# Kernel optimization log

Measured on AMD Instinct MI355X. Metric: run time of the kernel, lower is better.

The kernel has to match this reference:

```python
import jax, jax.numpy as jnp
import numpy as np

N_EVENTS = 8388608
H_DIM, W_DIM = 480, 640
BIN_WIDTH = 0.01
A_INIT = 1e-4  # initial a_x = a_y


def setup_inputs() -> dict:
    key = jax.random.key(0)
    k1, k2, k3, k4 = jax.random.split(key, 4)
    x = jax.random.uniform(k1, (N_EVENTS,), dtype=jnp.float32) * W_DIM
    y = jax.random.uniform(k2, (N_EVENTS,), dtype=jnp.float32) * H_DIM
    ts = jax.random.uniform(k3, (N_EVENTS,), dtype=jnp.float32)  # seconds in [0,1)
    pol = jnp.where(jax.random.bernoulli(k4, 0.5, (N_EVENTS,)), 1.0, -1.0).astype(jnp.float32)
    params = jnp.array([A_INIT, A_INIT], dtype=jnp.float32)
    # num_bins is data-dependent in the torch source (Python int from tensor min/max);
    # compute it here on concrete data so the jitted reference uses a static shape.
    t_w = ts - params[0] * x - params[1] * y
    num_bins = int((float(t_w.max()) - float(t_w.min())) / BIN_WIDTH) + 1
    return {
        'params': params,
        'x_coords': x, 'y_coords': y, 'timestamps': ts, 'polarities': pol,
        'H': H_DIM, 'W': W_DIM, 'bin_width': BIN_WIDTH, 'num_bins': num_bins,
    }


def _forward(params, x_coords, y_coords, timestamps, polarities, H, W, bin_width, num_bins):
    # warp: shift timestamps by learned scan parameters
    t_warped = timestamps - params[0] * x_coords - params[1] * y_coords
    t_start = t_warped.min()
    t_norm = (t_warped - t_start) / jnp.float32(bin_width)
    t0 = jnp.floor(t_norm)
    wt = t_norm - t0  # bilinear-in-time weight
    t0c = jnp.clip(t0, 0, num_bins - 1).astype(jnp.int32)
    t1c = jnp.clip(t0 + 1.0, 0, num_bins - 1).astype(jnp.int32)
    xi = x_coords.astype(jnp.int32)
    yi = y_coords.astype(jnp.int32)
    valid = (xi >= 0) & (xi < W) & (yi >= 0) & (yi < H)
    # masked-weight scatter == torch's boolean filtering before scatter_add
    vmask = valid.astype(jnp.float32)
    spatial = jnp.where(valid, yi * W + xi, 0)
    fi0 = t0c * (H * W) + spatial
    fi1 = t1c * (H * W) + spatial
    w0 = (1.0 - wt) * polarities * vmask
    w1 = wt * polarities * vmask
    num_elements = num_bins * H * W
    flat = jnp.zeros((num_elements,), dtype=jnp.float32)
    flat = flat.at[fi0].add(w0).at[fi1].add(w1)
    event_tensor = flat.reshape(num_bins, H, W)
    # torch.var is unbiased (ddof=1)
    variances = jnp.var(event_tensor.reshape(num_bins, -1), axis=1, ddof=1)
    loss = jnp.mean(variances)
    return event_tensor, loss


def reference(params, x_coords, y_coords, timestamps, polarities, H, W, bin_width, num_bins):
    return _forward(params, x_coords, y_coords, timestamps, polarities, H, W, bin_width, num_bins)
```

## Files before the change

kernel.cpp:

```cpp
#include <hip/hip_runtime.h>

#define W_ 640
#define H_ 480
#define HW_ (W_ * H_)
#define VAR_SPLIT 8
#define MAXNB_T 124
#define NBAND 120
#define NTK 40
#define NT3 (NBAND * NTK)
#define FB 48
#define FT 32
#define FB2 128
#define FT2 64
#define PAD 16
#define OVF 131072
#define CPB 8


__device__ __forceinline__ unsigned fkey(float f) {
    unsigned u = __float_as_uint(f);
    return (u & 0x80000000u) ? ~u : (u | 0x80000000u);
}
__device__ __forceinline__ float finv(unsigned k) {
    unsigned u = (k & 0x80000000u) ? (k ^ 0x80000000u) : ~k;
    return __uint_as_float(u);
}
__device__ __forceinline__ float warp_t(float ts, float xf, float yf, float p0, float p1) {
    return __fsub_rn(__fsub_rn(ts, __fmul_rn(p0, xf)), __fmul_rn(p1, yf));
}

__device__ __forceinline__ void spill_rec(unsigned r, int band,
                                          int* ovfcur, uint2* ovfrecs) {
    int j = atomicAdd(ovfcur, 1);
    if (j < OVF) {
        int tk = min((int)((r >> 18) & 63u), NTK - 1);
        int pix = (int)((r >> 12) & 63u);
        int yi = band * 4 + tk / 10;
        int xi = (tk % 10) * 64 + pix;
        int b = (int)((r >> 24) & 127u);
        float wt = __fmul_rn((float)(r & 4095u), 2.44140625e-4f);
        unsigned px = ((unsigned)b << 20) | (unsigned)(yi * W_ + xi) | (r & 0x80000000u);
        ovfrecs[j] = make_uint2(px, __float_as_uint(wt));
    }
}

__global__ void k_init(float* __restrict__ out, int n4, unsigned* __restrict__ minbits,
                       int* __restrict__ ovfcur, double* __restrict__ sums, int nsums,
                       int* __restrict__ curs, int ncur) {
    int tid = blockIdx.x * blockDim.x + threadIdx.x;
    int stride = gridDim.x * blockDim.x;
    float4* o4 = (float4*)out;
    float4 z = make_float4(0.f, 0.f, 0.f, 0.f);
    for (int i = tid; i < n4; i += stride) o4[i] = z;
    for (int i = tid; i < ncur; i += stride) curs[i] = 0;
    if (tid == 0) { *minbits = 0xFFFFFFFFu; *ovfcur = 0; }
    if (tid < nsums) sums[tid] = 0.0;
}

__global__ void k_min(const float* __restrict__ x, const float* __restrict__ y,
                      const float* __restrict__ ts, const float* __restrict__ params,
                      int n, unsigned* __restrict__ minbits) {
    float p0 = params[0], p1 = params[1];
    int tid = blockIdx.x * blockDim.x + threadIdx.x;
    int stride = gridDim.x * blockDim.x;
    int n4 = n >> 2;
    const float4* x4 = (const float4*)x;
    const float4* y4 = (const float4*)y;
    const float4* t4 = (const float4*)ts;
    unsigned k = 0xFFFFFFFFu;
    for (int i = tid; i < n4; i += stride) {
        float4 xv = x4[i], yv = y4[i], tv = t4[i];
        unsigned k0 = fkey(warp_t(tv.x, xv.x, yv.x, p0, p1));
        unsigned k1 = fkey(warp_t(tv.y, xv.y, yv.y, p0, p1));
        unsigned k2 = fkey(warp_t(tv.z, xv.z, yv.z, p0, p1));
        unsigned k3 = fkey(warp_t(tv.w, xv.w, yv.w, p0, p1));
        unsigned ka = min(k0, k1), kb = min(k2, k3);
        k = min(k, min(ka, kb));
    }
    for (int i = (n4 << 2) + tid; i < n; i += stride)
        k = min(k, fkey(warp_t(ts[i], x[i], y[i], p0, p1)));
    #pragma unroll
    for (int off = 32; off > 0; off >>= 1) {
        unsigned o = __shfl_down(k, off, 64);
        k = (o < k) ? o : k;
    }
    if ((threadIdx.x & 63) == 0) atomicMin(minbits, k);
}

__global__ void __launch_bounds__(256) k_pass1(
        const float* __restrict__ x, const float* __restrict__ y,
        const float* __restrict__ ts, const float* __restrict__ pol,
        const float* __restrict__ params, const float* __restrict__ bwp,
        int n, int nb, int cap1, int per, const unsigned* __restrict__ minbits,
        int* __restrict__ gcur, unsigned* __restrict__ recs1,
        int* __restrict__ ovfcur, uint2* __restrict__ ovfrecs) {
    __shared__ unsigned buf[NBAND][FB];
    __shared__ int cnt[NBAND];
    float p0 = params[0], p1 = params[1], bw = bwp[0];
    float tstart = finv(*minbits);
    float nbm1 = (float)(nb - 1);
    for (int t = threadIdx.x; t < NBAND; t += 256) cnt[t] = 0;
    __syncthreads();
    int lo = blockIdx.x * per;
    int hi = min(n, lo + per);
    int total = (hi > lo) ? (hi - lo) : 0;
    int nf4 = total >> 2;
    const float4* x4 = (const float4*)(x + lo);
    const float4* y4 = (const float4*)(y + lo);
    const float4* t4 = (const float4*)(ts + lo);
    const float4* p4 = (const float4*)(pol + lo);
    int wave = threadIdx.x >> 6, lane = threadIdx.x & 63;

    auto proc = [&](float xf, float yf, float tf, float pf) {
        int xi = (int)xf, yi = (int)yf;
        if (xi >= 0 && xi < W_ && yi >= 0 && yi < H_) {
            float tn = __fdiv_rn(__fsub_rn(warp_t(tf, xf, yf, p0, p1), tstart), bw);
            float t0f = floorf(tn);
            float wt = __fsub_rn(tn, t0f);
            int b = (int)fminf(fmaxf(t0f, 0.0f), nbm1);
            unsigned sgn = __float_as_uint(pf) & 0x80000000u;
            int band = yi >> 2;
            unsigned tk = (unsigned)((yi & 3) * 10 + (xi >> 6));
            unsigned pix = (unsigned)(xi & 63);
            unsigned wq = (unsigned)__fmul_rn(wt, 4096.0f);
            unsigned rec = sgn | ((unsigned)b << 24) | (tk << 18) | (pix << 12) | wq;
            int pos = atomicAdd(&cnt[band], 1);
            if (pos < FB) buf[band][pos] = rec;
            else {
                int j = atomicAdd(ovfcur, 1);
                if (j < OVF) {
                    unsigned px = ((unsigned)b << 20) | (unsigned)(yi * W_ + xi) | sgn;
                    ovfrecs[j] = make_uint2(px, __float_as_uint(wt));
                }
            }
        }
    };
    auto flush = [&](int thresh) {
        for (int bb = wave; bb < NBAND; bb += 4) {
            int c = min(cnt[bb], FB);
            if (c >= thresh) {
                int base = 0;
                if (lane == 0) base = atomicAdd(&gcur[bb * PAD], c);
                base = __shfl(base, 0, 64);
                for (int j = lane; j < c; j += 64) {
                    unsigned r = buf[bb][j];
                    int idx = base + j;
                    if (idx < cap1) recs1[(size_t)bb * cap1 + idx] = r;
                    else spill_rec(r, bb, ovfcur, ovfrecs);
                }
                if (lane == 0) cnt[bb] = 0;
            }
        }
    };

    int iters = (nf4 + 255) >> 8;
    for (int it = 0; it < iters; it++) {
        int i4 = (it << 8) + (int)threadIdx.x;
        bool valid = (i4 < nf4);
        float4 xv, yv, tv, pv;
        if (valid) { xv = x4[i4]; yv = y4[i4]; tv = t4[i4]; pv = p4[i4]; }
        if (valid) {
            proc(xv.x, yv.x, tv.x, pv.x);
            proc(xv.y, yv.y, tv.y, pv.y);
            proc(xv.z, yv.z, tv.z, pv.z);
            proc(xv.w, yv.w, tv.w, pv.w);
        }
        __syncthreads();
        flush(FT);
        __syncthreads();
    }
    int tbase = lo + (nf4 << 2);
    int trem = hi - tbase;
    if ((int)threadIdx.x < trem) {
        int i = tbase + (int)threadIdx.x;
        proc(x[i], y[i], ts[i], pol[i]);
    }
    __syncthreads();
    flush(1);
}

__global__ void __launch_bounds__(256) k_pass2(
        const unsigned* __restrict__ recs1, const int* __restrict__ gcur,
        int cap1, int cap2, int* __restrict__ tcur, unsigned* __restrict__ recs2,
        int* __restrict__ ovfcur, uint2* __restrict__ ovfrecs) {
    __shared__ unsigned buf[NTK][FB2];
    __shared__ int cnt[NTK];
    int band = blockIdx.x / CPB;
    int chunk = blockIdx.x % CPB;
    int c1 = min(gcur[band * PAD], cap1);
    int chunklen = (((c1 + CPB - 1) / CPB) + 3) & ~3;
    int start = chunk * chunklen;
    int end = min(start + chunklen, c1);
    const unsigned* seg = recs1 + (size_t)band * cap1;
    for (int t = threadIdx.x; t < NTK; t += 256) cnt[t] = 0;
    __syncthreads();
    int iters = (end > start) ? ((end - start + 1023) >> 10) : 0;
    int wave = threadIdx.x >> 6, lane = threadIdx.x & 63;
    for (int it = 0; it < iters; it++) {
        int idx = start + (it << 10) + (int)threadIdx.x * 4;
        unsigned r4[4];
        int m = 0;
        if (idx + 4 <= end) {
            uint4 q = *(const uint4*)&seg[idx];
            r4[0] = q.x; r4[1] = q.y; r4[2] = q.z; r4[3] = q.w; m = 4;
        } else {
            for (; idx + m < end && m < 4; m++) r4[m] = seg[idx + m];
        }
        #pragma unroll
        for (int k = 0; k < 4; k++) {
            if (k < m) {
                unsigned r = r4[k];
                int tx = min((int)((r >> 18) & 63u), NTK - 1);
                int pos = atomicAdd(&cnt[tx], 1);
                if (pos < FB2) buf[tx][pos] = r;
                else spill_rec(r, band, ovfcur, ovfrecs);
            }
        }
        __syncthreads();
        bool last = (it == iters - 1);
        for (int bb = wave; bb < NTK; bb += 4) {
            int c = min(cnt[bb], FB2);
            if (c >= (last ? 1 : FT2)) {
                int base = 0;
                if (lane == 0) base = atomicAdd(&tcur[(band * NTK + bb) * PAD], c);
                base = __shfl(base, 0, 64);
                for (int j = lane; j < c; j += 64) {
                    unsigned r = buf[bb][j];
                    int o = base + j;
                    if (o < cap2) recs2[(size_t)(band * NTK + bb) * cap2 + o] = r;
                    else spill_rec(r, band, ovfcur, ovfrecs);
                }
                if (lane == 0) cnt[bb] = 0;
            }
        }
        __syncthreads();
    }
}

__global__ void __launch_bounds__(256) k_accum6(
        const unsigned* __restrict__ recs2, const int* __restrict__ tcur,
        int nb, int cap2, float* __restrict__ out, double2* __restrict__ part2) {
    extern __shared__ float acc[];
    int T = blockIdx.x;
    int band = T / NTK, tk = T % NTK;
    int yy = band * 4 + tk / 10;
    int x0 = (tk % 10) * 64;
    int nacc4 = nb << 4;
    float4* acc4 = (float4*)acc;
    float4 z4 = make_float4(0.f, 0.f, 0.f, 0.f);
    for (int i = threadIdx.x; i < nacc4; i += 256) acc4[i] = z4;
    __syncthreads();
    int c2 = min(tcur[T * PAD], cap2);
    const unsigned* seg = recs2 + (size_t)T * cap2;
    int iters = (c2 + 1023) >> 10;
    for (int it = 0; it < iters; it++) {
        int idx = (it << 10) + (int)threadIdx.x * 4;
        unsigned r4[4];
        int m = 0;
        if (idx + 4 <= c2) {
            uint4 q = *(const uint4*)&seg[idx];
            r4[0] = q.x; r4[1] = q.y; r4[2] = q.z; r4[3] = q.w; m = 4;
        } else {
            for (; idx + m < c2 && m < 4; m++) r4[m] = seg[idx + m];
        }
        #pragma unroll
        for (int k = 0; k < 4; k++) {
            if (k < m) {
                unsigned r = r4[k];
                int b = min((int)((r >> 24) & 127u), nb - 1);
                int b1 = min(b + 1, nb - 1);
                int pix = (int)((r >> 12) & 63u);
                unsigned sgn = r & 0x80000000u;
                float wt = __fmul_rn((float)(r & 4095u), 2.44140625e-4f);
                float w0 = __uint_as_float(__float_as_uint(__fsub_rn(1.0f, wt)) ^ sgn);
                float w1 = __uint_as_float(__float_as_uint(wt) ^ sgn);
                atomicAdd(&acc[(b << 6) + pix], w0);
                atomicAdd(&acc[(b1 << 6) + pix], w1);
            }
        }
    }
    __syncthreads();
    size_t rowbase = (size_t)yy * W_ + x0;
    for (int i = threadIdx.x; i < nacc4; i += 256) {
        int b = i >> 4;
        int q = i & 15;
        *(float4*)&out[(size_t)b * HW_ + rowbase + (q << 2)] = acc4[i];
    }
    int t = threadIdx.x;
    if (t < 2 * nb) {
        int b = t >> 1, half = t & 1;
        double s = 0.0, ss = 0.0;
        int basei = (b << 6) + (half << 5);
        for (int jj = 0; jj < 32; jj++) {
            float v = acc[basei + ((jj + b) & 31)];
            double dv = (double)v;
            s += dv; ss += dv * dv;
        }
        part2[(size_t)T * (2 * nb) + t] = make_double2(s, ss);
    }
}

__global__ void __launch_bounds__(256) k_redsum(
        const double2* __restrict__ part2, int nb,
        double* __restrict__ sumv, double* __restrict__ sumsq) {
    int b = blockIdx.x;
    double s = 0.0, ss = 0.0;
    for (int i = threadIdx.x; i < NT3; i += 256) {
        double2 a = part2[(size_t)i * (2 * nb) + 2 * b];
        double2 c = part2[(size_t)i * (2 * nb) + 2 * b + 1];
        s += a.x + c.x; ss += a.y + c.y;
    }
    #pragma unroll
    for (int off = 32; off > 0; off >>= 1) {
        s += __shfl_down(s, off, 64);
        ss += __shfl_down(ss, off, 64);
    }
    __shared__ double sb[4], sb2[4];
    int wave = threadIdx.x >> 6, lane = threadIdx.x & 63;
    if (lane == 0) { sb[wave] = s; sb2[wave] = ss; }
    __syncthreads();
    if (threadIdx.x == 0) {
        for (int i = 1; i < 4; i++) { s += sb[i]; ss += sb2[i]; }
        sumv[b] = s; sumsq[b] = ss;
    }
}

__global__ void __launch_bounds__(256) k_accum2(
        const unsigned* __restrict__ recs1, const int* __restrict__ gcur,
        int nb, int cap1, float* __restrict__ out,
        double* __restrict__ sumv, double* __restrict__ sumsq) {
    extern __shared__ float acc[];
    int h = blockIdx.x;
    int xcd = h & 7;
    int j = h >> 3;
    int kk2 = j / NTK;
    int tk = j % NTK;
    int ry = xcd + 8 * kk2;
    int nacc = nb << 6;
    for (int i = threadIdx.x; i < nacc; i += 256) acc[i] = 0.f;
    __syncthreads();
    int c1 = min(gcur[ry * PAD], cap1);
    const unsigned* seg = recs1 + (size_t)ry * cap1;
    unsigned tku = (unsigned)tk;
    int iters = (c1 + 1023) >> 10;
    for (int it = 0; it < iters; it++) {
        int idx = (it << 10) + (int)threadIdx.x * 4;
        unsigned r4[4];
        int m = 0;
        if (idx + 4 <= c1) {
            uint4 q = *(const uint4*)&seg[idx];
            r4[0] = q.x; r4[1] = q.y; r4[2] = q.z; r4[3] = q.w; m = 4;
        } else {
            for (; idx + m < c1 && m < 4; m++) r4[m] = seg[idx + m];
        }
        #pragma unroll
        for (int k = 0; k < 4; k++) {
            if (k < m) {
                unsigned r = r4[k];
                if (((r >> 18) & 63u) == tku) {
                    int b = min((int)((r >> 24) & 127u), nb - 1);
                    int b1 = min(b + 1, nb - 1);
                    int pix = (int)((r >> 12) & 63u);
                    unsigned sgn = r & 0x80000000u;
                    float wt = __fmul_rn((float)(r & 4095u), 2.44140625e-4f);
                    float w0 = __uint_as_float(__float_as_uint(__fsub_rn(1.0f, wt)) ^ sgn);
                    float w1 = __uint_as_float(__float_as_uint(wt) ^ sgn);
                    atomicAdd(&acc[(b << 6) + pix], w0);
                    atomicAdd(&acc[(b1 << 6) + pix], w1);
                }
            }
        }
    }
    __syncthreads();
    int yy = ry * 4 + tk / 10;
    int x0 = (tk % 10) * 64;
    for (int i = threadIdx.x; i < nacc; i += 256) {
        int b = i >> 6, p = i & 63;
        out[(size_t)b * HW_ + (size_t)yy * W_ + x0 + p] = acc[i];
    }
    if ((int)threadIdx.x < nb) {
        int b = threadIdx.x;
        double s = 0.0, ss = 0.0;
        for (int j2 = 0; j2 < 64; j2++) {
            float v = acc[(b << 6) + ((j2 + b) & 63)];
            double dv = (double)v;
            s += dv; ss += dv * dv;
        }
        atomicAdd(&sumv[b], s);
        atomicAdd(&sumsq[b], ss);
    }
}

__global__ void k_ovf(const uint2* __restrict__ ovfrecs, const int* __restrict__ ovfcur,
                      int nb, float* __restrict__ out,
                      double* __restrict__ sumv, double* __restrict__ sumsq) {
    int m = min(*ovfcur, OVF);
    int tid = blockIdx.x * blockDim.x + threadIdx.x;
    int stride = gridDim.x * blockDim.x;
    for (int i = tid; i < m; i += stride) {
        uint2 r = ovfrecs[i];
        unsigned sgn = r.x & 0x80000000u;
        int b = (int)((r.x >> 20) & 511u);
        int sp = (int)(r.x & 0x7FFFFu);
        b = min(b, nb - 1); sp = min(sp, HW_ - 1);
        int b1 = min(b + 1, nb - 1);
        float wt = __uint_as_float(r.y);
        float w0 = __uint_as_float(__float_as_uint(__fsub_rn(1.0f, wt)) ^ sgn);
        float w1 = __uint_as_float(r.y ^ sgn);
        float o0 = unsafeAtomicAdd(out + (size_t)b * HW_ + sp, w0);
        atomicAdd(&sumv[b], (double)w0);
        atomicAdd(&sumsq[b], (double)w0 * ((double)w0 + 2.0 * (double)o0));
        float o1 = unsafeAtomicAdd(out + (size_t)b1 * HW_ + sp, w1);
        atomicAdd(&sumv[b1], (double)w1);
        atomicAdd(&sumsq[b1], (double)w1 * ((double)w1 + 2.0 * (double)o1));
    }
}

__global__ void k_scatter(const float* __restrict__ x, const float* __restrict__ y,
                          const float* __restrict__ ts, const float* __restrict__ pol,
                          const float* __restrict__ params, const float* __restrict__ bwp,
                          int n, int nb, const unsigned* __restrict__ minbits,
                          float* __restrict__ out) {
    float p0 = params[0], p1 = params[1];
    float bw = bwp[0];
    float tstart = finv(*minbits);
    float nbm1 = (float)(nb - 1);
    int tid = blockIdx.x * blockDim.x + threadIdx.x;
    int stride = gridDim.x * blockDim.x;
    for (int i = tid; i < n; i += stride) {
        float xf = x[i], yf = y[i];
        float tn = __fdiv_rn(__fsub_rn(warp_t(ts[i], xf, yf, p0, p1), tstart), bw);
        float t0f = floorf(tn);
        float wt = __fsub_rn(tn, t0f);
        int t0c = (int)fminf(fmaxf(t0f, 0.0f), nbm1);
        int t1c = (int)fminf(fmaxf(__fadd_rn(t0f, 1.0f), 0.0f), nbm1);
        int xi = (int)xf, yi = (int)yf;
        if (xi >= 0 && xi < W_ && yi >= 0 && yi < H_) {
            int sp = yi * W_ + xi;
            float p = pol[i];
            float w0 = __fmul_rn(__fsub_rn(1.0f, wt), p);
            float w1 = __fmul_rn(wt, p);
            unsafeAtomicAdd(&out[(size_t)t0c * HW_ + sp], w0);
            unsafeAtomicAdd(&out[(size_t)t1c * HW_ + sp], w1);
        }
    }
}

__global__ void k_sums(const float* __restrict__ out, double* __restrict__ sumv,
                       double* __restrict__ sumsq) {
    int b = blockIdx.x / VAR_SPLIT;
    int part = blockIdx.x % VAR_SPLIT;
    const int chunk = HW_ / VAR_SPLIT;
    const float* p = out + (size_t)b * HW_ + (size_t)part * chunk;
    double s = 0.0, ss = 0.0;
    for (int i = threadIdx.x; i < chunk; i += blockDim.x) {
        double v = (double)p[i];
        s += v; ss += v * v;
    }
    #pragma unroll
    for (int off = 32; off > 0; off >>= 1) {
        s += __shfl_down(s, off, 64);
        ss += __shfl_down(ss, off, 64);
    }
    __shared__ double sb[8], sb2[8];
    int wave = threadIdx.x >> 6, lane = threadIdx.x & 63;
    if (lane == 0) { sb[wave] = s; sb2[wave] = ss; }
    __syncthreads();
    if (threadIdx.x == 0) {
        int nw = blockDim.x >> 6;
        for (int i = 1; i < nw; i++) { s += sb[i]; ss += sb2[i]; }
        atomicAdd(&sumv[b], s);
        atomicAdd(&sumsq[b], ss);
    }
}

__global__ void k_final(const double* __restrict__ sumv, const double* __restrict__ sumsq,
                        int nb, float* __restrict__ loss) {
    double acc = 0.0;
    const double n = (double)HW_;
    for (int b = threadIdx.x; b < nb; b += blockDim.x) {
        double s = sumv[b], ss = sumsq[b];
        acc += (ss - s * s / n) / (n - 1.0);
    }
    #pragma unroll
    for (int off = 32; off > 0; off >>= 1) acc += __shfl_down(acc, off, 64);
    __shared__ double sb[8];
    int wave = threadIdx.x >> 6, lane = threadIdx.x & 63;
    if (lane == 0) sb[wave] = acc;
    __syncthreads();
    if (threadIdx.x == 0) {
        int nw = blockDim.x >> 6;
        for (int i = 1; i < nw; i++) acc += sb[i];
        *loss = (float)(acc / (double)nb);
    }
}

extern "C" void kernel_launch(void* const* d_in, const int* in_sizes, int n_in,
                              void* d_out, int out_size, void* d_ws, size_t ws_size,
                              hipStream_t stream) {
    const float* params = (const float*)d_in[0];
    const float* x      = (const float*)d_in[1];
    const float* y      = (const float*)d_in[2];
    const float* ts     = (const float*)d_in[3];
    const float* pol    = (const float*)d_in[4];
    const float* bwp    = (const float*)d_in[7];

    int n  = in_sizes[1];
    int nb = (out_size - 1) / HW_;
    float* out = (float*)d_out;

    size_t off_sums  = 128;
    size_t off_gcur  = (off_sums + 16ULL * nb + 63) & ~(size_t)63;
    size_t off_tcur  = off_gcur + 4ULL * NBAND * PAD;
    size_t off_part  = (off_tcur + 4ULL * NT3 * PAD + 63) & ~(size_t)63;
    size_t off_ovfr  = (off_part + 16ULL * 2 * nb * NT3 + 63) & ~(size_t)63;
    size_t off_recs1 = (off_ovfr + 8ULL * OVF + 63) & ~(size_t)63;

    unsigned* minbits = (unsigned*)d_ws;
    int*      ovfcur  = (int*)((char*)d_ws + 64);
    double*   sumv    = (double*)((char*)d_ws + off_sums);
    double*   sumsq   = sumv + nb;
    int*      gcur    = (int*)((char*)d_ws + off_gcur);
    int*      tcur    = (int*)((char*)d_ws + off_tcur);
    double2*  part2   = (double2*)((char*)d_ws + off_part);
    uint2*    ovfrecs = (uint2*)((char*)d_ws + off_ovfr);
    unsigned* recs1   = (unsigned*)((char*)d_ws + off_recs1);

    long long mean1 = (long long)n / NBAND;
    long long mean2 = (long long)n / NT3;

    long long cap1e = (mean1 + mean1 / 8 + 2048) & ~3LL;
    size_t off_recs2 = (off_recs1 + 4ULL * NBAND * cap1e + 63) & ~(size_t)63;
    unsigned* recs2 = (unsigned*)((char*)d_ws + off_recs2);
    long long avail2 = (ws_size > off_recs2)
                       ? (long long)((ws_size - off_recs2) / (4ULL * NT3)) : 0;
    long long cap2min = mean2 + mean2 / 8 + 128;
    long long cap2max = 2 * mean2 + 512;
    long long cap2ll = ((avail2 < cap2max) ? avail2 : cap2max) & ~3LL;
    bool exact = (n > 0) && (nb >= 1) && (nb <= MAXNB_T) && (cap2ll >= cap2min);

    long long avail1 = (ws_size > off_recs1)
                       ? (long long)((ws_size - off_recs1) / (4ULL * NBAND)) : 0;
    long long cap1f_max = 2 * mean1 + 4096;
    long long cap1fll = ((avail1 < cap1f_max) ? avail1 : cap1f_max) & ~3LL;
    bool filter = !exact && (n > 0) && (nb >= 1) && (nb <= MAXNB_T) &&
                  (cap1fll >= mean1 + mean1 / 12 + 2048);

    int cap1 = (int)(exact ? cap1e : cap1fll);
    int cap2 = (int)cap2ll;

    int n_tensor = nb * HW_;
    int n4 = (exact || filter) ? 0 : (n_tensor >> 2);

    const int BLK = 256;
    const int G1 = 1280;
    const int ITBLK = 1024;
    int per = (((n + G1 - 1) / G1) + ITBLK - 1) / ITBLK * ITBLK;
    int g1used = (n + per - 1) / per;

    hipLaunchKernelGGL(k_init, dim3(512), dim3(BLK), 0, stream,
                       out, n4, minbits, ovfcur, sumv, 2 * nb,
                       gcur, NBAND * PAD + NT3 * PAD);
    hipLaunchKernelGGL(k_min, dim3(2048), dim3(BLK), 0, stream,
                       x, y, ts, params, n, minbits);

    if (exact) {
        hipLaunchKernelGGL(k_pass1, dim3(g1used), dim3(BLK), 0, stream,
                           x, y, ts, pol, params, bwp, n, nb, cap1, per, minbits,
                           gcur, recs1, ovfcur, ovfrecs);
        hipLaunchKernelGGL(k_pass2, dim3(NBAND * CPB), dim3(BLK), 0, stream,
                           recs1, gcur, cap1, cap2, tcur, recs2, ovfcur, ovfrecs);
        hipLaunchKernelGGL(k_accum6, dim3(NT3), dim3(BLK), (size_t)nb * 64 * 4, stream,
                           recs2, tcur, nb, cap2, out, part2);
        hipLaunchKernelGGL(k_redsum, dim3(nb), dim3(BLK), 0, stream,
                           part2, nb, sumv, sumsq);
        hipLaunchKernelGGL(k_ovf, dim3(64), dim3(BLK), 0, stream,
                           ovfrecs, ovfcur, nb, out, sumv, sumsq);
    } else if (filter) {
        hipLaunchKernelGGL(k_pass1, dim3(g1used), dim3(BLK), 0, stream,
                           x, y, ts, pol, params, bwp, n, nb, cap1, per, minbits,
                           gcur, recs1, ovfcur, ovfrecs);
        hipLaunchKernelGGL(k_accum2, dim3(NT3), dim3(BLK), (size_t)nb * 64 * 4, stream,
                           recs1, gcur, nb, cap1, out, sumv, sumsq);
        hipLaunchKernelGGL(k_ovf, dim3(64), dim3(BLK), 0, stream,
                           ovfrecs, ovfcur, nb, out, sumv, sumsq);
    } else {
        hipLaunchKernelGGL(k_scatter, dim3(2048), dim3(BLK), 0, stream,
                           x, y, ts, pol, params, bwp, n, nb, minbits, out);
        hipLaunchKernelGGL(k_sums, dim3(nb * VAR_SPLIT), dim3(BLK), 0, stream,
                           out, sumv, sumsq);
    }

    hipLaunchKernelGGL(k_final, dim3(1), dim3(BLK), 0, stream,
                       sumv, sumsq, nb, out + n_tensor);
}
```

Before: 372.4 us.

## Bucket by time bin in pass2 and accumulate full 4-row bands per bin

Pass2 now splits each 4-row band's records by time bin rather than by 64-pixel tile. The accumulate kernel runs one block per (bin, band) with a 4x640 shared accumulator and pulls records from the current bin and the previous bin to add the w1 weights. The aim is a smaller shared footprint for better occupancy and fully contiguous output writes. The global atomicMin for the warped-time minimum becomes a two-stage block reduction, and the filter fallback path is removed. Each record is now read twice, and the smaller per-bin buffers may spill more records to the overflow path.

```diff
diff --git a/kernel.cpp b/kernel.cpp
--- a/kernel.cpp
+++ b/kernel.cpp
@@ -6,15 +6,14 @@
 #define VAR_SPLIT 8
 #define MAXNB_T 124
 #define NBAND 120
-#define NTK 40
-#define NT3 (NBAND * NTK)
 #define FB 48
 #define FT 32
-#define FB2 128
-#define FT2 64
+#define FB2 64
+#define FT2 32
 #define PAD 16
 #define OVF 131072
 #define CPB 8
+#define G0MIN 1280
 
 
 __device__ __forceinline__ unsigned fkey(float f) {
@@ -33,10 +32,9 @@
                                           int* ovfcur, uint2* ovfrecs) {
     int j = atomicAdd(ovfcur, 1);
     if (j < OVF) {
-        int tk = min((int)((r >> 18) & 63u), NTK - 1);
-        int pix = (int)((r >> 12) & 63u);
-        int yi = band * 4 + tk / 10;
-        int xi = (tk % 10) * 64 + pix;
+        int pix12 = (int)((r >> 12) & 4095u);
+        int yi = band * 4 + pix12 / W_;
+        int xi = pix12 % W_;
         int b = (int)((r >> 24) & 127u);
         float wt = __fmul_rn((float)(r & 4095u), 2.44140625e-4f);
         unsigned px = ((unsigned)b << 20) | (unsigned)(yi * W_ + xi) | (r & 0x80000000u);
@@ -57,9 +55,10 @@
     if (tid < nsums) sums[tid] = 0.0;
 }
 
-__global__ void k_min(const float* __restrict__ x, const float* __restrict__ y,
-                      const float* __restrict__ ts, const float* __restrict__ params,
-                      int n, unsigned* __restrict__ minbits) {
+__global__ void __launch_bounds__(256) k_min(
+        const float* __restrict__ x, const float* __restrict__ y,
+        const float* __restrict__ ts, const float* __restrict__ params,
+        int n, unsigned* __restrict__ minarr) {
     float p0 = params[0], p1 = params[1];
     int tid = blockIdx.x * blockDim.x + threadIdx.x;
     int stride = gridDim.x * blockDim.x;
@@ -74,17 +73,46 @@
         unsigned k1 = fkey(warp_t(tv.y, xv.y, yv.y, p0, p1));
         unsigned k2 = fkey(warp_t(tv.z, xv.z, yv.z, p0, p1));
         unsigned k3 = fkey(warp_t(tv.w, xv.w, yv.w, p0, p1));
-        unsigned ka = min(k0, k1), kb = min(k2, k3);
-        k = min(k, min(ka, kb));
+        k = min(k, min(min(k0, k1), min(k2, k3)));
     }
     for (int i = (n4 << 2) + tid; i < n; i += stride)
         k = min(k, fkey(warp_t(ts[i], x[i], y[i], p0, p1)));
     #pragma unroll
     for (int off = 32; off > 0; off >>= 1) {
         unsigned o = __shfl_down(k, off, 64);
-        k = (o < k) ? o : k;
-    }
-    if ((threadIdx.x & 63) == 0) atomicMin(minbits, k);
+        k = min(k, o);
+    }
+    __shared__ unsigned sb[4];
+    int wave = threadIdx.x >> 6, lane = threadIdx.x & 63;
+    if (lane == 0) sb[wave] = k;
+    __syncthreads();
+    if (threadIdx.x == 0) {
+        unsigned m = sb[0];
+        #pragma unroll
+        for (int i = 1; i < 4; i++) m = min(m, sb[i]);
+        minarr[blockIdx.x] = m;
+    }
+}
+
+__global__ void k_minred(const unsigned* __restrict__ minarr, int g,
+                         unsigned* __restrict__ minbits) {
+    unsigned k = 0xFFFFFFFFu;
+    for (int i = threadIdx.x; i < g; i += 256) k = min(k, minarr[i]);
+    #pragma unroll
+    for (int off = 32; off > 0; off >>= 1) {
+        unsigned o = __shfl_down(k, off, 64);
+        k = min(k, o);
+    }
+    __shared__ unsigned sb[4];
+    int wave = threadIdx.x >> 6, lane = threadIdx.x & 63;
+    if (lane == 0) sb[wave] = k;
+    __syncthreads();
+    if (threadIdx.x == 0) {
+        unsigned m = sb[0];
+        #pragma unroll
+        for (int i = 1; i < 4; i++) m = min(m, sb[i]);
+        *minbits = m;
+    }
 }
 
 __global__ void __launch_bounds__(256) k_pass1(
@@ -120,10 +148,9 @@
             int b = (int)fminf(fmaxf(t0f, 0.0f), nbm1);
             unsigned sgn = __float_as_uint(pf) & 0x80000000u;
             int band = yi >> 2;
-            unsigned tk = (unsigned)((yi & 3) * 10 + (xi >> 6));
-            unsigned pix = (unsigned)(xi & 63);
+            unsigned pix12 = (unsigned)((yi & 3) * W_ + xi);
             unsigned wq = (unsigned)__fmul_rn(wt, 4096.0f);
-            unsigned rec = sgn | ((unsigned)b << 24) | (tk << 18) | (pix << 12) | wq;
+            unsigned rec = sgn | ((unsigned)b << 24) | (pix12 << 12) | wq;
             int pos = atomicAdd(&cnt[band], 1);
             if (pos < FB) buf[band][pos] = rec;
             else {
@@ -181,10 +208,11 @@
 
 __global__ void __launch_bounds__(256) k_pass2(
         const unsigned* __restrict__ recs1, const int* __restrict__ gcur,
-        int cap1, int cap2, int* __restrict__ tcur, unsigned* __restrict__ recs2,
+        int nb, int cap1, int cap2, int* __restrict__ tcur,
+        unsigned* __restrict__ recs2,
         int* __restrict__ ovfcur, uint2* __restrict__ ovfrecs) {
-    __shared__ unsigned buf[NTK][FB2];
-    __shared__ int cnt[NTK];
+    __shared__ unsigned buf[MAXNB_T][FB2];
+    __shared__ int cnt[MAXNB_T];
     int band = blockIdx.x / CPB;
     int chunk = blockIdx.x % CPB;
     int c1 = min(gcur[band * PAD], cap1);
@@ -192,7 +220,7 @@
     int start = chunk * chunklen;
     int end = min(start + chunklen, c1);
     const unsigned* seg = recs1 + (size_t)band * cap1;
-    for (int t = threadIdx.x; t < NTK; t += 256) cnt[t] = 0;
+    for (int t = threadIdx.x; t < nb; t += 256) cnt[t] = 0;
     __syncthreads();
     int iters = (end > start) ? ((end - start + 1023) >> 10) : 0;
     int wave = threadIdx.x >> 6, lane = threadIdx.x & 63;
@@ -210,24 +238,24 @@
         for (int k = 0; k < 4; k++) {
             if (k < m) {
                 unsigned r = r4[k];
-                int tx = min((int)((r >> 18) & 63u), NTK - 1);
-                int pos = atomicAdd(&cnt[tx], 1);
-                if (pos < FB2) buf[tx][pos] = r;
+                int bi = min((int)((r >> 24) & 127u), nb - 1);
+                int pos = atomicAdd(&cnt[bi], 1);
+                if (pos < FB2) buf[bi][pos] = r;
                 else spill_rec(r, band, ovfcur, ovfrecs);
             }
         }
         __syncthreads();
         bool last = (it == iters - 1);
-        for (int bb = wave; bb < NTK; bb += 4) {
+        for (int bb = wave; bb < nb; bb += 4) {
             int c = min(cnt[bb], FB2);
             if (c >= (last ? 1 : FT2)) {
                 int base = 0;
-                if (lane == 0) base = atomicAdd(&tcur[(band * NTK + bb) * PAD], c);
+                if (lane == 0) base = atomicAdd(&tcur[(band * nb + bb) * PAD], c);
                 base = __shfl(base, 0, 64);
                 for (int j = lane; j < c; j += 64) {
                     unsigned r = buf[bb][j];
                     int o = base + j;
-                    if (o < cap2) recs2[(size_t)(band * NTK + bb) * cap2 + o] = r;
+                    if (o < cap2) recs2[(size_t)(band * nb + bb) * cap2 + o] = r;
                     else spill_rec(r, band, ovfcur, ovfrecs);
                 }
                 if (lane == 0) cnt[bb] = 0;
@@ -237,157 +265,102 @@
     }
 }
 
-__global__ void __launch_bounds__(256) k_accum6(
+__global__ void __launch_bounds__(256) k_accum8(
         const unsigned* __restrict__ recs2, const int* __restrict__ tcur,
-        int nb, int cap2, float* __restrict__ out, double2* __restrict__ part2) {
-    extern __shared__ float acc[];
-    int T = blockIdx.x;
-    int band = T / NTK, tk = T % NTK;
-    int yy = band * 4 + tk / 10;
-    int x0 = (tk % 10) * 64;
-    int nacc4 = nb << 4;
+        int nb, int cap2, float* __restrict__ out, double2* __restrict__ part) {
+    __shared__ float acc[4 * W_];
+    __shared__ double sb[4], sb2[4];
+    int blk = blockIdx.x;
+    int band = blk % NBAND;
+    int b = blk / NBAND;
     float4* acc4 = (float4*)acc;
     float4 z4 = make_float4(0.f, 0.f, 0.f, 0.f);
-    for (int i = threadIdx.x; i < nacc4; i += 256) acc4[i] = z4;
-    __syncthreads();
-    int c2 = min(tcur[T * PAD], cap2);
-    const unsigned* seg = recs2 + (size_t)T * cap2;
-    int iters = (c2 + 1023) >> 10;
-    for (int it = 0; it < iters; it++) {
-        int idx = (it << 10) + (int)threadIdx.x * 4;
-        unsigned r4[4];
-        int m = 0;
-        if (idx + 4 <= c2) {
-            uint4 q = *(const uint4*)&seg[idx];
-            r4[0] = q.x; r4[1] = q.y; r4[2] = q.z; r4[3] = q.w; m = 4;
-        } else {
-            for (; idx + m < c2 && m < 4; m++) r4[m] = seg[idx + m];
-        }
-        #pragma unroll
-        for (int k = 0; k < 4; k++) {
-            if (k < m) {
-                unsigned r = r4[k];
-                int b = min((int)((r >> 24) & 127u), nb - 1);
-                int b1 = min(b + 1, nb - 1);
-                int pix = (int)((r >> 12) & 63u);
-                unsigned sgn = r & 0x80000000u;
-                float wt = __fmul_rn((float)(r & 4095u), 2.44140625e-4f);
-                float w0 = __uint_as_float(__float_as_uint(__fsub_rn(1.0f, wt)) ^ sgn);
-                float w1 = __uint_as_float(__float_as_uint(wt) ^ sgn);
-                atomicAdd(&acc[(b << 6) + pix], w0);
-                atomicAdd(&acc[(b1 << 6) + pix], w1);
+    for (int i = threadIdx.x; i < 640; i += 256) acc4[i] = z4;
+    __syncthreads();
+
+    auto apply = [&](const unsigned* seg, int c, bool addw0, bool addw1) {
+        int iters = (c + 1023) >> 10;
+        for (int it = 0; it < iters; it++) {
+            int idx = (it << 10) + (int)threadIdx.x * 4;
+            unsigned r4[4];
+            int m = 0;
+            if (idx + 4 <= c) {
+                uint4 q = *(const uint4*)&seg[idx];
+                r4[0] = q.x; r4[1] = q.y; r4[2] = q.z; r4[3] = q.w; m = 4;
+            } else {
+                for (; idx + m < c && m < 4; m++) r4[m] = seg[idx + m];
             }
-        }
-    }
-    __syncthreads();
-    size_t rowbase = (size_t)yy * W_ + x0;
-    for (int i = threadIdx.x; i < nacc4; i += 256) {
-        int b = i >> 4;
-        int q = i & 15;
-        *(float4*)&out[(size_t)b * HW_ + rowbase + (q << 2)] = acc4[i];
-    }
-    int t = threadIdx.x;
-    if (t < 2 * nb) {
-        int b = t >> 1, half = t & 1;
-        double s = 0.0, ss = 0.0;
-        int basei = (b << 6) + (half << 5);
-        for (int jj = 0; jj < 32; jj++) {
-            float v = acc[basei + ((jj + b) & 31)];
-            double dv = (double)v;
-            s += dv; ss += dv * dv;
-        }
-        part2[(size_t)T * (2 * nb) + t] = make_double2(s, ss);
-    }
-}
-
-__global__ void __launch_bounds__(256) k_redsum(
-        const double2* __restrict__ part2, int nb,
-        double* __restrict__ sumv, double* __restrict__ sumsq) {
-    int b = blockIdx.x;
+            #pragma unroll
+            for (int k = 0; k < 4; k++) {
+                if (k < m) {
+                    unsigned r = r4[k];
+                    int pix = min((int)((r >> 12) & 4095u), 4 * W_ - 1);
+                    unsigned sgn = r & 0x80000000u;
+                    float wt = __fmul_rn((float)(r & 4095u), 2.44140625e-4f);
+                    if (addw0) {
+                        float w0 = __uint_as_float(__float_as_uint(__fsub_rn(1.0f, wt)) ^ sgn);
+                        atomicAdd(&acc[pix], w0);
+                    }
+                    if (addw1) {
+                        float w1 = __uint_as_float(__float_as_uint(wt) ^ sgn);
+                        atomicAdd(&acc[pix], w1);
+                    }
+                }
+            }
+        }
+    };
+
+    int base = band * nb;
+    int cb = min(tcur[(base + b) * PAD], cap2);
+    apply(recs2 + (size_t)(base + b) * cap2, cb, true, b == nb - 1);
+    if (b > 0) {
+        int cm = min(tcur[(base + b - 1) * PAD], cap2);
+        apply(recs2 + (size_t)(base + b - 1) * cap2, cm, false, true);
+    }
+    __syncthreads();
+    float4* dst4 = (float4*)(out + (size_t)b * HW_ + (size_t)band * 4 * W_);
+    for (int i = threadIdx.x; i < 640; i += 256) dst4[i] = acc4[i];
     double s = 0.0, ss = 0.0;
-    for (int i = threadIdx.x; i < NT3; i += 256) {
-        double2 a = part2[(size_t)i * (2 * nb) + 2 * b];
-        double2 c = part2[(size_t)i * (2 * nb) + 2 * b + 1];
-        s += a.x + c.x; ss += a.y + c.y;
+    for (int i = threadIdx.x; i < 4 * W_; i += 256) {
+        double v = (double)acc[i];
+        s += v; ss += v * v;
     }
     #pragma unroll
     for (int off = 32; off > 0; off >>= 1) {
         s += __shfl_down(s, off, 64);
         ss += __shfl_down(ss, off, 64);
     }
+    int wave = threadIdx.x >> 6, lane = threadIdx.x & 63;
+    if (lane == 0) { sb[wave] = s; sb2[wave] = ss; }
+    __syncthreads();
+    if (threadIdx.x == 0) {
+        #pragma unroll
+        for (int i = 1; i < 4; i++) { s += sb[i]; ss += sb2[i]; }
+        part[(size_t)b * NBAND + band] = make_double2(s, ss);
+    }
+}
+
+__global__ void k_redsum(const double2* __restrict__ part, int nb,
+                         double* __restrict__ sumv, double* __restrict__ sumsq) {
+    int b = blockIdx.x;
+    double s = 0.0, ss = 0.0;
+    for (int i = threadIdx.x; i < NBAND; i += 256) {
+        double2 a = part[(size_t)b * NBAND + i];
+        s += a.x; ss += a.y;
+    }
+    #pragma unroll
+    for (int off = 32; off > 0; off >>= 1) {
+        s += __shfl_down(s, off, 64);
+        ss += __shfl_down(ss, off, 64);
+    }
     __shared__ double sb[4], sb2[4];
     int wave = threadIdx.x >> 6, lane = threadIdx.x & 63;
     if (lane == 0) { sb[wave] = s; sb2[wave] = ss; }
     __syncthreads();
     if (threadIdx.x == 0) {
+        #pragma unroll
         for (int i = 1; i < 4; i++) { s += sb[i]; ss += sb2[i]; }
-        sumv[b] = s; sumsq[b] = ss;
-    }
-}
-
-__global__ void __launch_bounds__(256) k_accum2(
-        const unsigned* __restrict__ recs1, const int* __restrict__ gcur,
-        int nb, int cap1, float* __restrict__ out,
-        double* __restrict__ sumv, double* __restrict__ sumsq) {
-    extern __shared__ float acc[];
-    int h = blockIdx.x;
-    int xcd = h & 7;
-    int j = h >> 3;
-    int kk2 = j / NTK;
-    int tk = j % NTK;
-    int ry = xcd + 8 * kk2;
-    int nacc = nb << 6;
-    for (int i = threadIdx.x; i < nacc; i += 256) acc[i] = 0.f;
-    __syncthreads();
-    int c1 = min(gcur[ry * PAD], cap1);
-    const unsigned* seg = recs1 + (size_t)ry * cap1;
-    unsigned tku = (unsigned)tk;
-    int iters = (c1 + 1023) >> 10;
-    for (int it = 0; it < iters; it++) {
-        int idx = (it << 10) + (int)threadIdx.x * 4;
-        unsigned r4[4];
-        int m = 0;
-        if (idx + 4 <= c1) {
-            uint4 q = *(const uint4*)&seg[idx];
-            r4[0] = q.x; r4[1] = q.y; r4[2] = q.z; r4[3] = q.w; m = 4;
-        } else {
-            for (; idx + m < c1 && m < 4; m++) r4[m] = seg[idx + m];
-        }
-        #pragma unroll
-        for (int k = 0; k < 4; k++) {
-            if (k < m) {
-                unsigned r = r4[k];
-                if (((r >> 18) & 63u) == tku) {
-                    int b = min((int)((r >> 24) & 127u), nb - 1);
-                    int b1 = min(b + 1, nb - 1);
-                    int pix = (int)((r >> 12) & 63u);
-                    unsigned sgn = r & 0x80000000u;
-                    float wt = __fmul_rn((float)(r & 4095u), 2.44140625e-4f);
-                    float w0 = __uint_as_float(__float_as_uint(__fsub_rn(1.0f, wt)) ^ sgn);
-                    float w1 = __uint_as_float(__float_as_uint(wt) ^ sgn);
-                    atomicAdd(&acc[(b << 6) + pix], w0);
-                    atomicAdd(&acc[(b1 << 6) + pix], w1);
-                }
-            }
-        }
-    }
-    __syncthreads();
-    int yy = ry * 4 + tk / 10;
-    int x0 = (tk % 10) * 64;
-    for (int i = threadIdx.x; i < nacc; i += 256) {
-        int b = i >> 6, p = i & 63;
-        out[(size_t)b * HW_ + (size_t)yy * W_ + x0 + p] = acc[i];
-    }
-    if ((int)threadIdx.x < nb) {
-        int b = threadIdx.x;
-        double s = 0.0, ss = 0.0;
-        for (int j2 = 0; j2 < 64; j2++) {
-            float v = acc[(b << 6) + ((j2 + b) & 63)];
-            double dv = (double)v;
-            s += dv; ss += dv * dv;
-        }
-        atomicAdd(&sumv[b], s);
-        atomicAdd(&sumsq[b], ss);
+        sumv[b] += s; sumsq[b] += ss;
     }
 }
 
@@ -510,47 +483,43 @@
     float* out = (float*)d_out;
 
     size_t off_sums  = 128;
-    size_t off_gcur  = (off_sums + 16ULL * nb + 63) & ~(size_t)63;
+    size_t off_mina  = (off_sums + 16ULL * nb + 63) & ~(size_t)63;
+    size_t off_gcur  = (off_mina + 4ULL * G0MIN + 63) & ~(size_t)63;
     size_t off_tcur  = off_gcur + 4ULL * NBAND * PAD;
-    size_t off_part  = (off_tcur + 4ULL * NT3 * PAD + 63) & ~(size_t)63;
-    size_t off_ovfr  = (off_part + 16ULL * 2 * nb * NT3 + 63) & ~(size_t)63;
+    size_t off_part  = (off_tcur + 4ULL * NBAND * nb * PAD + 63) & ~(size_t)63;
+    size_t off_ovfr  = (off_part + 16ULL * nb * NBAND + 63) & ~(size_t)63;
     size_t off_recs1 = (off_ovfr + 8ULL * OVF + 63) & ~(size_t)63;
 
     unsigned* minbits = (unsigned*)d_ws;
     int*      ovfcur  = (int*)((char*)d_ws + 64);
     double*   sumv    = (double*)((char*)d_ws + off_sums);
     double*   sumsq   = sumv + nb;
+    unsigned* minarr  = (unsigned*)((char*)d_ws + off_mina);
     int*      gcur    = (int*)((char*)d_ws + off_gcur);
     int*      tcur    = (int*)((char*)d_ws + off_tcur);
-    double2*  part2   = (double2*)((char*)d_ws + off_part);
+    double2*  part    = (double2*)((char*)d_ws + off_part);
     uint2*    ovfrecs = (uint2*)((char*)d_ws + off_ovfr);
     unsigned* recs1   = (unsigned*)((char*)d_ws + off_recs1);
 
-    long long mean1 = (long long)n / NBAND;
-    long long mean2 = (long long)n / NT3;
+    long long mean1  = (long long)n / NBAND;
+    long long mean2b = (nb >= 1) ? ((long long)n / ((long long)NBAND * nb)) : 0;
 
     long long cap1e = (mean1 + mean1 / 8 + 2048) & ~3LL;
     size_t off_recs2 = (off_recs1 + 4ULL * NBAND * cap1e + 63) & ~(size_t)63;
     unsigned* recs2 = (unsigned*)((char*)d_ws + off_recs2);
+    long long denom = 4LL * NBAND * (nb >= 1 ? nb : 1);
     long long avail2 = (ws_size > off_recs2)
-                       ? (long long)((ws_size - off_recs2) / (4ULL * NT3)) : 0;
-    long long cap2min = mean2 + mean2 / 8 + 128;
-    long long cap2max = 2 * mean2 + 512;
+                       ? (long long)((ws_size - off_recs2) / denom) : 0;
+    long long cap2min = mean2b + mean2b / 8 + 128;
+    long long cap2max = 2 * mean2b + 512;
     long long cap2ll = ((avail2 < cap2max) ? avail2 : cap2max) & ~3LL;
     bool exact = (n > 0) && (nb >= 1) && (nb <= MAXNB_T) && (cap2ll >= cap2min);
 
-    long long avail1 = (ws_size > off_recs1)
-                       ? (long long)((ws_size - off_recs1) / (4ULL * NBAND)) : 0;
-    long long cap1f_max = 2 * mean1 + 4096;
-    long long cap1fll = ((avail1 < cap1f_max) ? avail1 : cap1f_max) & ~3LL;
-    bool filter = !exact && (n > 0) && (nb >= 1) && (nb <= MAXNB_T) &&
-                  (cap1fll >= mean1 + mean1 / 12 + 2048);
-
-    int cap1 = (int)(exact ? cap1e : cap1fll);
+    int cap1 = (int)cap1e;
     int cap2 = (int)cap2ll;
 
     int n_tensor = nb * HW_;
-    int n4 = (exact || filter) ? 0 : (n_tensor >> 2);
+    int n4 = exact ? 0 : (n_tensor >> 2);
 
     const int BLK = 256;
     const int G1 = 1280;
@@ -558,30 +527,25 @@
     int per = (((n + G1 - 1) / G1) + ITBLK - 1) / ITBLK * ITBLK;
     int g1used = (n + per - 1) / per;
 
+    int ncur = NBAND * PAD + NBAND * nb * PAD;
+
     hipLaunchKernelGGL(k_init, dim3(512), dim3(BLK), 0, stream,
-                       out, n4, minbits, ovfcur, sumv, 2 * nb,
-                       gcur, NBAND * PAD + NT3 * PAD);
-    hipLaunchKernelGGL(k_min, dim3(2048), dim3(BLK), 0, stream,
-                       x, y, ts, params, n, minbits);
+                       out, n4, minbits, ovfcur, sumv, 2 * nb, gcur, ncur);
+    hipLaunchKernelGGL(k_min, dim3(G0MIN), dim3(BLK), 0, stream,
+                       x, y, ts, params, n, minarr);
+    hipLaunchKernelGGL(k_minred, dim3(1), dim3(BLK), 0, stream,
+                       minarr, G0MIN, minbits);
 
     if (exact) {
         hipLaunchKernelGGL(k_pass1, dim3(g1used), dim3(BLK), 0, stream,
                            x, y, ts, pol, params, bwp, n, nb, cap1, per, minbits,
                            gcur, recs1, ovfcur, ovfrecs);
         hipLaunchKernelGGL(k_pass2, dim3(NBAND * CPB), dim3(BLK), 0, stream,
-                           recs1, gcur, cap1, cap2, tcur, recs2, ovfcur, ovfrecs);
-        hipLaunchKernelGGL(k_accum6, dim3(NT3), dim3(BLK), (size_t)nb * 64 * 4, stream,
-                           recs2, tcur, nb, cap2, out, part2);
+                           recs1, gcur, nb, cap1, cap2, tcur, recs2, ovfcur, ovfrecs);
+        hipLaunchKernelGGL(k_accum8, dim3(nb * NBAND), dim3(BLK), 0, stream,
+                           recs2, tcur, nb, cap2, out, part);
         hipLaunchKernelGGL(k_redsum, dim3(nb), dim3(BLK), 0, stream,
-                           part2, nb, sumv, sumsq);
-        hipLaunchKernelGGL(k_ovf, dim3(64), dim3(BLK), 0, stream,
-                           ovfrecs, ovfcur, nb, out, sumv, sumsq);
-    } else if (filter) {
-        hipLaunchKernelGGL(k_pass1, dim3(g1used), dim3(BLK), 0, stream,
-                           x, y, ts, pol, params, bwp, n, nb, cap1, per, minbits,
-                           gcur, recs1, ovfcur, ovfrecs);
-        hipLaunchKernelGGL(k_accum2, dim3(NT3), dim3(BLK), (size_t)nb * 64 * 4, stream,
-                           recs1, gcur, nb, cap1, out, sumv, sumsq);
+                           part, nb, sumv, sumsq);
         hipLaunchKernelGGL(k_ovf, dim3(64), dim3(BLK), 0, stream,
                            ovfrecs, ovfcur, nb, out, sumv, sumsq);
     } else {
```

New measurement: 316.4 us. -15.0%, faster.
